# Optimization experiments

Hardware: AMD Instinct MI355X
Metric: run time of the kernel (lower is better)

Reference implementation:

```python
import jax, jax.numpy as jnp
import numpy as np

N, IN_C, OUT_C = 4096, 256, 64
ALPHA = 0.2  # LeakyReLU negative slope


def setup_inputs() -> dict:
    key = jax.random.key(0)
    k1, k2, k3, k4 = jax.random.split(key, 4)
    H = jax.random.normal(k1, (N, IN_C), dtype=jnp.float32)
    adj = jax.random.randint(k2, (N, N), 0, 2, dtype=jnp.int32)
    # xavier_uniform with gain=1.414
    gain = 1.414
    limW = gain * np.sqrt(6.0 / (IN_C + OUT_C))
    W = jax.random.uniform(k3, (IN_C, OUT_C), minval=-limW, maxval=limW, dtype=jnp.float32)
    lima = gain * np.sqrt(6.0 / (2 * OUT_C + 1))
    a = jax.random.uniform(k4, (2 * OUT_C, 1), minval=-lima, maxval=lima, dtype=jnp.float32)
    return {"H": H, "adj": adj, "W": W, "a": a}


def reference(H, adj, W, a):
    Wh = H @ W  # [N, out_C]
    # Attention_Mat[i,j] = concat(Wh_i, Wh_j); score = Attention_Mat @ a
    # = (Wh @ a1)_i + (Wh @ a2)_j  -- fused, avoids the O(N^2 * 2F) tensor.
    a1, a2 = a[:OUT_C, 0], a[OUT_C:, 0]
    e = (Wh @ a1)[:, None] + (Wh @ a2)[None, :]  # [N, N]
    e = jnp.where(e > 0, e, ALPHA * e)  # LeakyReLU
    att = jax.nn.softmax(e, axis=1)
    # NOTE: original masks AFTER softmax (rows are not renormalized).
    att = jnp.where(adj > 0, att, jnp.zeros_like(att))
    out = att @ Wh  # [N, out_C]
    return jax.nn.elu(out)  # concat=True
```

## Files before the change

kernel.cpp:

```cpp
#include <hip/hip_runtime.h>
#include <math.h>

static constexpr int NN   = 4096;
static constexpr int INC  = 256;
static constexpr int OUTC = 64;

typedef _Float16 half8 __attribute__((ext_vector_type(8)));
typedef float floatx4 __attribute__((ext_vector_type(4)));

__device__ __forceinline__ float lrelu(float x) {
    return fmaxf(x, 0.f) + 0.2f * fminf(x, 0.f);
}
__device__ __forceinline__ float elu1(float x) {
    return x > 0.f ? x : (__expf(x) - 1.f);
}

__global__ __launch_bounds__(256) void k_wh(const float* __restrict__ H,
                                            const float* __restrict__ W,
                                            const float* __restrict__ a,
                                            unsigned short* __restrict__ WhT,
                                            float* __restrict__ f1,
                                            float* __restrict__ f2) {
    __shared__ __align__(16) float Hl[16 * INC];
    __shared__ _Float16 Tl[16 * 68];
    const int t = threadIdx.x;
    const int i0 = blockIdx.x * 16;
    {
        const float4* H4 = (const float4*)(H + i0 * INC);
        float4* Hl4 = (float4*)Hl;
        #pragma unroll
        for (int u = 0; u < 4; ++u) Hl4[u * 256 + t] = H4[u * 256 + t];
    }
    __syncthreads();
    const int c = t & 63;
    const int g = t >> 6;
    const float a1c = a[c];
    const float a2c = a[OUTC + c];
    float acc[4] = {0.f, 0.f, 0.f, 0.f};
    const float4* Hl4 = (const float4*)Hl;
    #pragma unroll 4
    for (int k4 = 0; k4 < INC / 4; ++k4) {
        const float w0 = W[(k4 * 4 + 0) * OUTC + c];
        const float w1 = W[(k4 * 4 + 1) * OUTC + c];
        const float w2 = W[(k4 * 4 + 2) * OUTC + c];
        const float w3 = W[(k4 * 4 + 3) * OUTC + c];
        #pragma unroll
        for (int s = 0; s < 4; ++s) {
            const float4 h = Hl4[(g + 4 * s) * (INC / 4) + k4];
            acc[s] = fmaf(h.x, w0, fmaf(h.y, w1, fmaf(h.z, w2, fmaf(h.w, w3, acc[s]))));
        }
    }
    #pragma unroll
    for (int s = 0; s < 4; ++s) {
        const int r = g + 4 * s;
        Tl[r * 68 + c] = (_Float16)acc[s];
        float v1 = acc[s] * a1c;
        float v2 = acc[s] * a2c;
        #pragma unroll
        for (int off = 32; off; off >>= 1) {
            v1 += __shfl_xor(v1, off);
            v2 += __shfl_xor(v2, off);
        }
        if (c == 0) { f1[i0 + r] = v1; f2[i0 + r] = v2; }
    }
    __syncthreads();
    const int c2 = t >> 2;
    const int rs = (t & 3) * 4;
    ushort4 u;
    u.x = *(const unsigned short*)&Tl[(rs + 0) * 68 + c2];
    u.y = *(const unsigned short*)&Tl[(rs + 1) * 68 + c2];
    u.z = *(const unsigned short*)&Tl[(rs + 2) * 68 + c2];
    u.w = *(const unsigned short*)&Tl[(rs + 3) * 68 + c2];
    *(ushort4*)(WhT + c2 * NN + i0 + rs) = u;
}

__global__ __launch_bounds__(1024, 4) void k_att(const int* __restrict__ adj,
                                                 const _Float16* __restrict__ WhT,
                                                 const float* __restrict__ f1,
                                                 const float* __restrict__ f2,
                                                 float* __restrict__ out) {
    __shared__ __align__(16) float sf2[NN];
    __shared__ __align__(16) float sacc[16 * 1024];
    __shared__ __align__(8) unsigned long long smask[2][16][9];
    __shared__ float sden[16 * 16];
    __shared__ float smax[16];
    const int t = threadIdx.x;
    const int w = t >> 6;
    const int l = t & 63;
    const int m = l & 15;
    const int quad = l >> 4;
    const int i0 = blockIdx.x * 16;

    {
        const float4 v = ((const float4*)f2)[t];
        ((float4*)sf2)[t] = v;
        float mloc = fmaxf(fmaxf(v.x, v.y), fmaxf(v.z, v.w));
        #pragma unroll
        for (int off = 32; off; off >>= 1) mloc = fmaxf(mloc, __shfl_xor(mloc, off));
        if (l == 0) smax[w] = mloc;
    }

    const int* arow = adj + (size_t)(i0 + w) * NN;
    int pv[8];
    #pragma unroll
    for (int e = 0; e < 8; ++e) pv[e] = arow[e * 64 + l];
    #pragma unroll
    for (int e = 0; e < 8; ++e) {
        const unsigned long long bm = __ballot(pv[e] > 0);
        if (l == 0) smask[0][w][e] = bm;
    }
    __syncthreads();

    float maxf2 = smax[0];
    #pragma unroll
    for (int k = 1; k < 16; ++k) maxf2 = fmaxf(maxf2, smax[k]);
    const float f1r = f1[i0 + m];
    const float mrow = lrelu(f1r + maxf2);

    float den = 0.f;
    floatx4 acc[4] = {{0.f,0.f,0.f,0.f},{0.f,0.f,0.f,0.f},{0.f,0.f,0.f,0.f},{0.f,0.f,0.f,0.f}};
    const int jb = w * 32 + quad * 8;
    const unsigned char* mbase = (const unsigned char*)&smask[0][0][0]
                               + m * 72 + (w >> 1) * 8 + (w & 1) * 4 + quad;

    for (int tt = 0; tt < 8; ++tt) {
        if (tt < 7) {
            #pragma unroll
            for (int e = 0; e < 8; ++e) pv[e] = arow[(tt + 1) * 512 + e * 64 + l];
        }
        const int j = tt * 512 + jb;
        const unsigned int mb = mbase[(tt & 1) * (16 * 72)];
        const float4 g0 = *(const float4*)(sf2 + j);
        const float4 g1 = *(const float4*)(sf2 + j + 4);
        half8 af;
        {
            float p;
            p = __expf(lrelu(f1r + g0.x) - mrow); den += p; af[0] = (mb & 1u)   ? (_Float16)p : (_Float16)0.f;
            p = __expf(lrelu(f1r + g0.y) - mrow); den += p; af[1] = (mb & 2u)   ? (_Float16)p : (_Float16)0.f;
            p = __expf(lrelu(f1r + g0.z) - mrow); den += p; af[2] = (mb & 4u)   ? (_Float16)p : (_Float16)0.f;
            p = __expf(lrelu(f1r + g0.w) - mrow); den += p; af[3] = (mb & 8u)   ? (_Float16)p : (_Float16)0.f;
            p = __expf(lrelu(f1r + g1.x) - mrow); den += p; af[4] = (mb & 16u)  ? (_Float16)p : (_Float16)0.f;
            p = __expf(lrelu(f1r + g1.y) - mrow); den += p; af[5] = (mb & 32u)  ? (_Float16)p : (_Float16)0.f;
            p = __expf(lrelu(f1r + g1.z) - mrow); den += p; af[6] = (mb & 64u)  ? (_Float16)p : (_Float16)0.f;
            p = __expf(lrelu(f1r + g1.w) - mrow); den += p; af[7] = (mb & 128u) ? (_Float16)p : (_Float16)0.f;
        }
        #pragma unroll
        for (int nt = 0; nt < 4; ++nt) {
            const half8 bf = *(const half8*)(WhT + (size_t)(nt * 16 + m) * NN + j);
            acc[nt] = __builtin_amdgcn_mfma_f32_16x16x32_f16(af, bf, acc[nt], 0, 0, 0);
        }
        if (tt < 7) {
            #pragma unroll
            for (int e = 0; e < 8; ++e) {
                const unsigned long long bm = __ballot(pv[e] > 0);
                if (l == 0) smask[(tt + 1) & 1][w][e] = bm;
            }
        }
        __syncthreads();
    }

    den += __shfl_xor(den, 16);
    den += __shfl_xor(den, 32);
    if (l < 16) sden[w * 16 + l] = den;
    #pragma unroll
    for (int nt = 0; nt < 4; ++nt)
        #pragma unroll
        for (int r = 0; r < 4; ++r)
            sacc[w * 1024 + (quad * 4 + r) * 64 + nt * 16 + m] = acc[nt][r];
    __syncthreads();
    float s = 0.f;
    #pragma unroll
    for (int w2 = 0; w2 < 16; ++w2) s += sacc[w2 * 1024 + t];
    float dden = 0.f;
    const int orow = t >> 6;
    #pragma unroll
    for (int w2 = 0; w2 < 16; ++w2) dden += sden[w2 * 16 + orow];
    out[(size_t)i0 * OUTC + t] = elu1(s / dden);
}

extern "C" void kernel_launch(void* const* d_in, const int* in_sizes, int n_in,
                              void* d_out, int out_size, void* d_ws, size_t ws_size,
                              hipStream_t stream) {
    const float* H  = (const float*)d_in[0];
    const int* adj  = (const int*)d_in[1];
    const float* W  = (const float*)d_in[2];
    const float* a  = (const float*)d_in[3];
    float* out = (float*)d_out;
    char* ws = (char*)d_ws;
    unsigned short* WhT = (unsigned short*)(ws);
    float* f1 = (float*)(ws + (512 << 10));
    float* f2 = (float*)(ws + (528 << 10));
    hipLaunchKernelGGL(k_wh,  dim3(256), dim3(256),  0, stream, H, W, a, WhT, f1, f2);
    hipLaunchKernelGGL(k_att, dim3(256), dim3(1024), 0, stream,
                       adj, (const _Float16*)WhT, f1, f2, out);
}
```

Baseline: 127.5 us.

## Give each wave a contiguous column slab and keep adjacency masks in registers

Each wave now owns a contiguous 256-column slab and loads all 16 rows of adj for it up front with int4 loads. It ballots these into per-lane 64-bit mask registers, so the shared-memory mask double buffer and the per-iteration __syncthreads in the main loop go away. The intent is to remove block-wide barriers and LDS mask traffic from the exp/MFMA loop. In exchange, all adj loads happen before compute with no overlap, and the j-ordering of the partial sums changes.

```diff
diff --git a/kernel.cpp b/kernel.cpp
--- a/kernel.cpp
+++ b/kernel.cpp
@@ -81,7 +81,6 @@
                                                  float* __restrict__ out) {
     __shared__ __align__(16) float sf2[NN];
     __shared__ __align__(16) float sacc[16 * 1024];
-    __shared__ __align__(8) unsigned long long smask[2][16][9];
     __shared__ float sden[16 * 16];
     __shared__ float smax[16];
     const int t = threadIdx.x;
@@ -90,6 +89,7 @@
     const int m = l & 15;
     const int quad = l >> 4;
     const int i0 = blockIdx.x * 16;
+    const int J0 = w * 256;
 
     {
         const float4 v = ((const float4*)f2)[t];
@@ -100,14 +100,18 @@
         if (l == 0) smax[w] = mloc;
     }
 
-    const int* arow = adj + (size_t)(i0 + w) * NN;
-    int pv[8];
-    #pragma unroll
-    for (int e = 0; e < 8; ++e) pv[e] = arow[e * 64 + l];
-    #pragma unroll
-    for (int e = 0; e < 8; ++e) {
-        const unsigned long long bm = __ballot(pv[e] > 0);
-        if (l == 0) smask[0][w][e] = bm;
+    unsigned long long mw0 = 0, mw1 = 0, mw2 = 0, mw3 = 0;
+    {
+        const int* abase = adj + (size_t)i0 * NN + J0 + l * 4;
+        #pragma unroll 4
+        for (int r = 0; r < 16; ++r) {
+            const int4 av = *(const int4*)(abase + (size_t)r * NN);
+            const unsigned long long b0 = __ballot(av.x > 0);
+            const unsigned long long b1 = __ballot(av.y > 0);
+            const unsigned long long b2 = __ballot(av.z > 0);
+            const unsigned long long b3 = __ballot(av.w > 0);
+            if (m == r) { mw0 = b0; mw1 = b1; mw2 = b2; mw3 = b3; }
+        }
     }
     __syncthreads();
 
@@ -119,46 +123,31 @@
 
     float den = 0.f;
     floatx4 acc[4] = {{0.f,0.f,0.f,0.f},{0.f,0.f,0.f,0.f},{0.f,0.f,0.f,0.f},{0.f,0.f,0.f,0.f}};
-    const int jb = w * 32 + quad * 8;
-    const unsigned char* mbase = (const unsigned char*)&smask[0][0][0]
-                               + m * 72 + (w >> 1) * 8 + (w & 1) * 4 + quad;
 
-    for (int tt = 0; tt < 8; ++tt) {
-        if (tt < 7) {
-            #pragma unroll
-            for (int e = 0; e < 8; ++e) pv[e] = arow[(tt + 1) * 512 + e * 64 + l];
-        }
-        const int j = tt * 512 + jb;
-        const unsigned int mb = mbase[(tt & 1) * (16 * 72)];
+    #pragma unroll 2
+    for (int s = 0; s < 8; ++s) {
+        const int j = J0 + s * 32 + quad * 8;
+        const unsigned int ub = s * 8 + quad * 2;
         const float4 g0 = *(const float4*)(sf2 + j);
         const float4 g1 = *(const float4*)(sf2 + j + 4);
         half8 af;
         {
             float p;
-            p = __expf(lrelu(f1r + g0.x) - mrow); den += p; af[0] = (mb & 1u)   ? (_Float16)p : (_Float16)0.f;
-            p = __expf(lrelu(f1r + g0.y) - mrow); den += p; af[1] = (mb & 2u)   ? (_Float16)p : (_Float16)0.f;
-            p = __expf(lrelu(f1r + g0.z) - mrow); den += p; af[2] = (mb & 4u)   ? (_Float16)p : (_Float16)0.f;
-            p = __expf(lrelu(f1r + g0.w) - mrow); den += p; af[3] = (mb & 8u)   ? (_Float16)p : (_Float16)0.f;
-            p = __expf(lrelu(f1r + g1.x) - mrow); den += p; af[4] = (mb & 16u)  ? (_Float16)p : (_Float16)0.f;
-            p = __expf(lrelu(f1r + g1.y) - mrow); den += p; af[5] = (mb & 32u)  ? (_Float16)p : (_Float16)0.f;
-            p = __expf(lrelu(f1r + g1.z) - mrow); den += p; af[6] = (mb & 64u)  ? (_Float16)p : (_Float16)0.f;
-            p = __expf(lrelu(f1r + g1.w) - mrow); den += p; af[7] = (mb & 128u) ? (_Float16)p : (_Float16)0.f;
+            p = __expf(lrelu(f1r + g0.x) - mrow); den += p; af[0] = ((mw0 >> ub)       & 1ull) ? (_Float16)p : (_Float16)0.f;
+            p = __expf(lrelu(f1r + g0.y) - mrow); den += p; af[1] = ((mw1 >> ub)       & 1ull) ? (_Float16)p : (_Float16)0.f;
+            p = __expf(lrelu(f1r + g0.z) - mrow); den += p; af[2] = ((mw2 >> ub)       & 1ull) ? (_Float16)p : (_Float16)0.f;
+            p = __expf(lrelu(f1r + g0.w) - mrow); den += p; af[3] = ((mw3 >> ub)       & 1ull) ? (_Float16)p : (_Float16)0.f;
+            p = __expf(lrelu(f1r + g1.x) - mrow); den += p; af[4] = ((mw0 >> (ub + 1)) & 1ull) ? (_Float16)p : (_Float16)0.f;
+            p = __expf(lrelu(f1r + g1.y) - mrow); den += p; af[5] = ((mw1 >> (ub + 1)) & 1ull) ? (_Float16)p : (_Float16)0.f;
+            p = __expf(lrelu(f1r + g1.z) - mrow); den += p; af[6] = ((mw2 >> (ub + 1)) & 1ull) ? (_Float16)p : (_Float16)0.f;
+            p = __expf(lrelu(f1r + g1.w) - mrow); den += p; af[7] = ((mw3 >> (ub + 1)) & 1ull) ? (_Float16)p : (_Float16)0.f;
         }
         #pragma unroll
         for (int nt = 0; nt < 4; ++nt) {
             const half8 bf = *(const half8*)(WhT + (size_t)(nt * 16 + m) * NN + j);
             acc[nt] = __builtin_amdgcn_mfma_f32_16x16x32_f16(af, bf, acc[nt], 0, 0, 0);
         }
-        if (tt < 7) {
-            #pragma unroll
-            for (int e = 0; e < 8; ++e) {
-                const unsigned long long bm = __ballot(pv[e] > 0);
-                if (l == 0) smask[(tt + 1) & 1][w][e] = bm;
-            }
-        }
-        __syncthreads();
     }
-
     den += __shfl_xor(den, 16);
     den += __shfl_xor(den, 32);
     if (l < 16) sden[w * 16 + l] = den;
```

After: 126.9 us. Within noise of the previous version (-0.5%).
